# Kernel optimization log

Measured on AMD Instinct MI355X. Metric: run time of the kernel, lower is better.

Reference implementation:

```python
import jax, jax.numpy as jnp
import numpy as np

B, K, D = 65536, 1024, 256
COMMITMENT_COST = 0.25


def setup_inputs() -> dict:
    key = jax.random.key(0)
    kz, kw = jax.random.split(key)
    z = jax.random.normal(kz, (B, D), dtype=jnp.float32)
    # torch init: uniform_(-1/num_embeddings, 1/num_embeddings)
    weight = jax.random.uniform(kw, (K, D), dtype=jnp.float32,
                                minval=-1.0 / K, maxval=1.0 / K)
    return {"z": z, "weight": weight}


def reference(z, weight):
    # squared L2 distances via expansion: ||z||^2 - 2 z.e + ||e||^2  -> [B, K]
    dists = (jnp.sum(z * z, axis=1, keepdims=True)
             - 2.0 * (z @ weight.T)
             + jnp.sum(weight * weight, axis=1))
    indices = jnp.argmin(dists, axis=1)          # [B]
    z_q = weight[indices]                         # [B, D] gather

    sg_z = jax.lax.stop_gradient(z)
    mse = jnp.mean((z_q - sg_z) ** 2)
    commitment_loss = COMMITMENT_COST * mse      # F.mse_loss(z.detach(), z_q)
    vq_loss = mse + commitment_loss              # F.mse_loss(z_q, z.detach()) + commitment

    # straight-through estimator
    z_q_st = z + jax.lax.stop_gradient(z_q - z)
    return z_q_st, vq_loss, indices
```

## Files before the change

kernel.cpp:

```cpp
#include <hip/hip_runtime.h>
#include <math.h>

#define B_N 65536
#define K_N 1024
#define D_N 256
#define CAPW 512
#define NWV 8

typedef __attribute__((ext_vector_type(8))) short bf16x8;
typedef __attribute__((ext_vector_type(4))) float f32x4;

__device__ __forceinline__ unsigned short f2bf(float f) {
    unsigned u = __float_as_uint(f);
    return (unsigned short)((u + 0x7FFFu + ((u >> 16) & 1u)) >> 16);
}
__device__ __forceinline__ unsigned encf(float f) {
    unsigned u = __float_as_uint(f);
    return u ^ ((unsigned)((int)u >> 31) | 0x80000000u);
}
__device__ __forceinline__ float decf(unsigned e) {
    unsigned u = (e & 0x80000000u) ? (e ^ 0x80000000u) : ~e;
    return __uint_as_float(u);
}

__device__ __forceinline__ float chain_dot(const float* __restrict__ zp,
                                           const float* __restrict__ wp) {
    float acc = 0.0f;
    #pragma unroll 1
    for (int j = 0; j < 64; ++j) {
        float4 za = *reinterpret_cast<const float4*>(zp + (j << 2));
        float4 wa = *reinterpret_cast<const float4*>(wp + (j << 2));
        acc = fmaf(za.x, wa.x, acc);
        acc = fmaf(za.y, wa.y, acc);
        acc = fmaf(za.z, wa.z, acc);
        acc = fmaf(za.w, wa.w, acc);
    }
    return acc;
}

__device__ __forceinline__ int pA(int i, int k) {
    return ((i + k) & 15) - 7 + 9 * ((k >> 4) & 1);
}
__device__ __forceinline__ int pB(int j, int k) {
    return ((j + 3 * k) & 15) - 7 + 5 * ((k >> 4) & 1);
}

__global__ void mfma_probe_kernel(int* __restrict__ flag) {
    const int l = threadIdx.x & 63;
    const int c15 = l & 15, g = l >> 4;
    bf16x8 afr[8], bfr[8];
    #pragma unroll
    for (int m = 0; m < 8; ++m)
        #pragma unroll
        for (int e = 0; e < 8; ++e) {
            const int k = m * 32 + g * 8 + e;
            afr[m][e] = (short)f2bf((float)pA(c15, k));
            bfr[m][e] = (short)f2bf((float)pB(c15, k));
        }
    f32x4 acc = {0.f, 0.f, 0.f, 0.f};
    #pragma unroll
    for (int m = 0; m < 8; ++m)
        acc = __builtin_amdgcn_mfma_f32_16x16x32_bf16(afr[m], bfr[m], acc, 0, 0, 0);
    int h1 = 1, h2 = 1;
    #pragma unroll 1
    for (int reg = 0; reg < 4; ++reg) {
        const int q = 4 * g + reg;
        int e1 = 0, e2 = 0;
        for (int k = 0; k < 32; ++k) {
            e1 += pA(q, k) * pB(c15, k);
            e2 += pA(c15, k) * pB(q, k);
        }
        e1 *= 8; e2 *= 8;
        if (acc[reg] != (float)e1) h1 = 0;
        if (acc[reg] != (float)e2) h2 = 0;
    }
    h1 = __all(h1); h2 = __all(h2);
    if (threadIdx.x == 0) *flag = h1 ? 0 : (h2 ? 1 : 2);
}

__global__ void wprep_kernel(const float* __restrict__ w,
                             float* __restrict__ ww,
                             unsigned short* __restrict__ wb) {
    int wave = (int)((blockIdx.x * blockDim.x + threadIdx.x) >> 6);
    int lane = threadIdx.x & 63;
    if (wave >= K_N) return;
    const float4 v = *reinterpret_cast<const float4*>(w + ((size_t)wave << 8) + (lane << 2));
    float s = v.x * v.x + v.y * v.y + v.z * v.z + v.w * v.w;
    #pragma unroll
    for (int off = 32; off; off >>= 1) s += __shfl_xor(s, off, 64);
    if (lane == 0) ww[wave] = s;
    ushort4 b;
    b.x = f2bf(v.x); b.y = f2bf(v.y); b.z = f2bf(v.z); b.w = f2bf(v.w);
    const int mp = lane >> 3;
    const int gp = (lane >> 1) & 3;
    const int hp = (wave >> 4) & 1;
    const size_t off_b = (size_t)(wave >> 5) * 16384
        + (size_t)(((hp * 8 + mp) * 64 + gp * 16 + (wave & 15)) * 16)
        + (size_t)((lane & 1) * 8);
    *reinterpret_cast<ushort4*>((char*)wb + off_b) = b;
}

__global__ __launch_bounds__(512, 4)
void vq_mfma_kernel(const float* __restrict__ z, const float* __restrict__ w,
                    const unsigned short* __restrict__ wb,
                    const float* __restrict__ ww,
                    const int* __restrict__ flagp,
                    float* __restrict__ zq_out,
                    float* __restrict__ idxf_out,
                    double* __restrict__ partial) {
    __shared__ float wwlds[1024];
    __shared__ unsigned short rc[NWV][CAPW];
    __shared__ unsigned short dqv[NWV][CAPW];
    __shared__ float zz_l[NWV][16], band_l[NWV][16], thrm[NWV][16];
    __shared__ unsigned rowminU[NWV][16];
    __shared__ unsigned long long bestk[NWV][16];
    __shared__ double wsum[NWV];

    const int tid = threadIdx.x;
    const int wv = tid >> 6, l = tid & 63;
    const int c15 = l & 15, g = l >> 4;
    const int b0 = blockIdx.x << 7;
    const int rbase = b0 + (wv << 4);
    const int flag = flagp[0];
    const bool fb0 = !(flag == 0 || flag == 1);

    if (l < 16) {
        rowminU[wv][l] = 0xFFFFFFFFu;
        bestk[wv][l]   = ~0ull;
    }
    reinterpret_cast<float2*>(wwlds)[tid] = reinterpret_cast<const float2*>(ww)[tid];

    bool fbw = fb0;
    int n = 0;

    int ml[4], cl[4];
    #pragma unroll
    for (int reg = 0; reg < 4; ++reg) {
        if (flag == 1) { ml[reg] = c15;          cl[reg] = 4 * g + reg; }
        else           { ml[reg] = 4 * g + reg;  cl[reg] = c15;         }
    }

    bf16x8 afr[8];
    {
        const float* zr = z + ((size_t)(rbase + c15) << 8) + (g << 3);
        float s = 0.0f, a = 0.0f;
        #pragma unroll
        for (int m = 0; m < 8; ++m) {
            float4 lo = *reinterpret_cast<const float4*>(zr + (m << 5));
            float4 hi = *reinterpret_cast<const float4*>(zr + (m << 5) + 4);
            s += lo.x * lo.x + lo.y * lo.y + lo.z * lo.z + lo.w * lo.w;
            s += hi.x * hi.x + hi.y * hi.y + hi.z * hi.z + hi.w * hi.w;
            a += fabsf(lo.x) + fabsf(lo.y) + fabsf(lo.z) + fabsf(lo.w);
            a += fabsf(hi.x) + fabsf(hi.y) + fabsf(hi.z) + fabsf(hi.w);
            bf16x8 f;
            f[0] = (short)f2bf(lo.x); f[1] = (short)f2bf(lo.y);
            f[2] = (short)f2bf(lo.z); f[3] = (short)f2bf(lo.w);
            f[4] = (short)f2bf(hi.x); f[5] = (short)f2bf(hi.y);
            f[6] = (short)f2bf(hi.z); f[7] = (short)f2bf(hi.w);
            afr[m] = f;
        }
        s += __shfl_xor(s, 16, 64);
        s += __shfl_xor(s, 32, 64);
        a += __shfl_xor(a, 16, 64);
        a += __shfl_xor(a, 32, 64);
        if (g == 0) {
            zz_l[wv][c15]   = s;
            band_l[wv][c15] = a * 2.0e-5f + 1.0e-3f;
        }
    }

    __syncthreads();

    float zzv[4], bdv[4];
    #pragma unroll
    for (int reg = 0; reg < 4; ++reg) {
        zzv[reg] = zz_l[wv][ml[reg]];
        bdv[reg] = band_l[wv][ml[reg]];
    }

    float runmin[4] = {INFINITY, INFINITY, INFINITY, INFINITY};
    int base = 0;

    const char* wbL = (const char*)wb + (l << 4);

#define PROCESS(ACC, TC, DOCOL, DOFM)                                         \
    _Pragma("unroll")                                                         \
    for (int reg = 0; reg < 4; ++reg) {                                       \
        const int _code = ((TC) << 5) + (h << 4) + cl[reg];                   \
        const float _dist = (zzv[reg] - 2.0f * (ACC)[reg]) + wwlds[_code];    \
        if (DOCOL) {                                                          \
            const bool _pred = (_dist <= runmin[reg] + bdv[reg]);             \
            const unsigned long long _mask = __ballot(_pred);                 \
            if (_mask) {                                                      \
                if (_pred) {                                                  \
                    const int _slot = base + (int)__popcll(_mask & ((1ull << l) - 1ull)); \
                    if (_slot < CAPW) {                                       \
                        rc[wv][_slot] = (unsigned short)((ml[reg] << 10) | _code); \
                        union { _Float16 h16; unsigned short u; } _cv;        \
                        _cv.h16 = (_Float16)(_dist - zzv[reg]);               \
                        dqv[wv][_slot] = _cv.u;                               \
                    }                                                         \
                }                                                             \
                base += (int)__popcll(_mask);                                 \
            }                                                                 \
        }                                                                     \
        if (DOFM) runmin[reg] = fminf(runmin[reg], _dist);                    \
    }

#define MINSYNC()                                                             \
    if (flag == 1) {                                                          \
        _Pragma("unroll")                                                     \
        for (int reg = 0; reg < 4; ++reg) {                                   \
            runmin[reg] = fminf(runmin[reg], __shfl_xor(runmin[reg], 16, 64)); \
            runmin[reg] = fminf(runmin[reg], __shfl_xor(runmin[reg], 32, 64)); \
        }                                                                     \
    } else {                                                                  \
        _Pragma("unroll")                                                     \
        for (int reg = 0; reg < 4; ++reg) {                                   \
            runmin[reg] = fminf(runmin[reg], __shfl_xor(runmin[reg], 1, 64)); \
            runmin[reg] = fminf(runmin[reg], __shfl_xor(runmin[reg], 2, 64)); \
            runmin[reg] = fminf(runmin[reg], __shfl_xor(runmin[reg], 4, 64)); \
            runmin[reg] = fminf(runmin[reg], __shfl_xor(runmin[reg], 8, 64)); \
        }                                                                     \
    }

    if (!fb0) {
        #pragma unroll 1
        for (int t = 0; t < 32; ++t) {
            const char* tp = wbL + t * 16384;
            #pragma unroll
            for (int h = 0; h < 2; ++h) {
                bf16x8 bfr[8];
                #pragma unroll
                for (int m = 0; m < 8; ++m)
                    bfr[m] = *reinterpret_cast<const bf16x8*>(tp + (h << 13) + (m << 10));
                f32x4 acc = {0.f, 0.f, 0.f, 0.f};
                #pragma unroll
                for (int m = 0; m < 8; ++m)
                    acc = __builtin_amdgcn_mfma_f32_16x16x32_bf16(afr[m], bfr[m], acc, 0, 0, 0);
                if (t > 0) { PROCESS(acc, t, 1, 1) }
                else       { PROCESS(acc, t, 0, 1) }
            }
            MINSYNC()
        }

        {
            const char* tp = wbL;
            #pragma unroll
            for (int h = 0; h < 2; ++h) {
                bf16x8 bfr[8];
                #pragma unroll
                for (int m = 0; m < 8; ++m)
                    bfr[m] = *reinterpret_cast<const bf16x8*>(tp + (h << 13) + (m << 10));
                f32x4 acc = {0.f, 0.f, 0.f, 0.f};
                #pragma unroll
                for (int m = 0; m < 8; ++m)
                    acc = __builtin_amdgcn_mfma_f32_16x16x32_bf16(afr[m], bfr[m], acc, 0, 0, 0);
                PROCESS(acc, 0, 1, 0)
            }
        }

        n = base;
        if (n > CAPW) fbw = true;

        #pragma unroll
        for (int reg = 0; reg < 4; ++reg)
            atomicMin(&rowminU[wv][ml[reg]], encf(runmin[reg]));
        if (l < 16)
            thrm[wv][l] = (decf(rowminU[wv][l]) + band_l[wv][l]) - zz_l[wv][l] + 4.0e-4f;
    }
#undef PROCESS
#undef MINSYNC

    if (!fbw) {
        int viol = 0;
        #pragma unroll 1
        for (int i = l; i < n; i += 64) {
            const int e = rc[wv][i];
            const int m = e >> 10, code = e & 1023;
            union { _Float16 h16; unsigned short u; } cv;
            cv.u = dqv[wv][i];
            const float dval = (float)cv.h16;
            if (dval <= thrm[wv][m]) {
                const float dot = chain_dot(z + ((size_t)(rbase + m) << 8),
                                            w + ((size_t)code << 8));
                const float dist = (zz_l[wv][m] - 2.0f * dot) + wwlds[code];
                if (fabsf((dval + zz_l[wv][m]) - dist) > band_l[wv][m] + 4.0e-4f)
                    viol = 1;
                atomicMin(&bestk[wv][m],
                          ((unsigned long long)encf(dist) << 32) | (unsigned)code);
            }
        }
        if (__any(viol)) fbw = true;
    }
    if (fbw) {
        #pragma unroll 1
        for (int m = 0; m < 16; ++m) {
            const float zzm = zz_l[wv][m];
            const float* zp = z + ((size_t)(rbase + m) << 8);
            for (int code = l; code < 1024; code += 64) {
                const float dist = (zzm - 2.0f * chain_dot(zp, w + ((size_t)code << 8)))
                                 + wwlds[code];
                atomicMin(&bestk[wv][m],
                          ((unsigned long long)encf(dist) << 32) | (unsigned)code);
            }
        }
    }

    if (l < 16) {
        const int code = (int)(unsigned)(bestk[wv][l] & 0xFFFFFFFFull);
        idxf_out[rbase + l] = (float)code;
    }

    int codes[16];
    #pragma unroll
    for (int rr = 0; rr < 16; ++rr)
        codes[rr] = (int)(unsigned)(bestk[wv][rr] & 0xFFFFFFFFull);
    #pragma unroll 4
    for (int rr = 0; rr < 16; ++rr) {
        const float4 wv4 = *reinterpret_cast<const float4*>(
            w + ((size_t)codes[rr] << 8) + (l << 2));
        *reinterpret_cast<float4*>(
            zq_out + ((size_t)(rbase + rr) << 8) + (l << 2)) = wv4;
    }

    double s = 0.0;
    if (l < 16) s = (double)decf((unsigned)(bestk[wv][l] >> 32));
    #pragma unroll
    for (int off = 8; off; off >>= 1) s += __shfl_xor(s, off, 64);
    if (l == 0) wsum[wv] = s;
    __syncthreads();
    if (tid == 0) {
        double t = 0.0;
        #pragma unroll
        for (int i = 0; i < NWV; ++i) t += wsum[i];
        partial[blockIdx.x] = t;
    }
}

__global__ void finalize_loss_kernel(const double* __restrict__ partial,
                                     float* __restrict__ out) {
    __shared__ double sd[256];
    const int t = threadIdx.x;
    double s = 0.0;
    for (int i = t; i < 512; i += 256) s += partial[i];
    sd[t] = s;
    __syncthreads();
    #pragma unroll
    for (int off = 128; off; off >>= 1) {
        if (t < off) sd[t] += sd[t + off];
        __syncthreads();
    }
    if (t == 0) {
        double mse = sd[0] / ((double)B_N * (double)D_N);
        out[0] = (float)(mse * 1.25);
    }
}

extern "C" void kernel_launch(void* const* d_in, const int* in_sizes, int n_in,
                              void* d_out, int out_size, void* d_ws, size_t ws_size,
                              hipStream_t stream) {
    const float* z = (const float*)d_in[0];
    const float* w = (const float*)d_in[1];

    float* out  = (float*)d_out;
    float* zq   = out;
    float* loss = out + (size_t)B_N * D_N;
    float* idxf = loss + 1;

    char* wsb = (char*)d_ws;
    float*          ww      = (float*)(wsb);
    unsigned short* wb      = (unsigned short*)(wsb + 4096);
    int*            flag    = (int*)(wsb + 528384);
    double*         partial = (double*)(wsb + 528448);

    mfma_probe_kernel<<<1, 64, 0, stream>>>(flag);

    wprep_kernel<<<K_N / 4, 256, 0, stream>>>(w, ww, wb);

    vq_mfma_kernel<<<B_N / 128, 512, 0, stream>>>(z, w, wb, ww, flag,
                                                  zq, idxf, partial);

    finalize_loss_kernel<<<1, 256, 0, stream>>>(partial, loss);
}
```

Before: 188.9 us.

## Split codebook across wave pairs and halve rows per block

Each pair of waves now shares the same 16 z rows, with each wave scanning one half of the codebook. Per-row minimums and best codes are merged through shared-memory atomics, with added block barriers. Each block covers 64 rows, so the grid doubles to give more resident blocks per CU and better latency hiding. In exchange, each z row is loaded and converted to bf16 twice. The per-wave running minimum sees only half the codes, so the filter is looser and may keep more candidates.

```diff
diff --git a/kernel.cpp b/kernel.cpp
--- a/kernel.cpp
+++ b/kernel.cpp
@@ -111,22 +111,24 @@
     __shared__ float wwlds[1024];
     __shared__ unsigned short rc[NWV][CAPW];
     __shared__ unsigned short dqv[NWV][CAPW];
-    __shared__ float zz_l[NWV][16], band_l[NWV][16], thrm[NWV][16];
-    __shared__ unsigned rowminU[NWV][16];
-    __shared__ unsigned long long bestk[NWV][16];
-    __shared__ double wsum[NWV];
+    __shared__ float zz_l[4][16], band_l[4][16], thrm[4][16];
+    __shared__ unsigned rowminU[4][16];
+    __shared__ unsigned long long bestk[4][16];
+    __shared__ double wsum[4];
 
     const int tid = threadIdx.x;
     const int wv = tid >> 6, l = tid & 63;
+    const int wv2 = wv >> 1;
+    const int kh = wv & 1;
     const int c15 = l & 15, g = l >> 4;
-    const int b0 = blockIdx.x << 7;
-    const int rbase = b0 + (wv << 4);
+    const int b0 = blockIdx.x << 6;
+    const int rbase = b0 + (wv2 << 4);
     const int flag = flagp[0];
     const bool fb0 = !(flag == 0 || flag == 1);
 
-    if (l < 16) {
-        rowminU[wv][l] = 0xFFFFFFFFu;
-        bestk[wv][l]   = ~0ull;
+    if (kh == 0 && l < 16) {
+        rowminU[wv2][l] = 0xFFFFFFFFu;
+        bestk[wv2][l]   = ~0ull;
     }
     reinterpret_cast<float2*>(wwlds)[tid] = reinterpret_cast<const float2*>(ww)[tid];
 
@@ -164,8 +166,8 @@
         a += __shfl_xor(a, 16, 64);
         a += __shfl_xor(a, 32, 64);
         if (g == 0) {
-            zz_l[wv][c15]   = s;
-            band_l[wv][c15] = a * 2.0e-5f + 1.0e-3f;
+            zz_l[wv2][c15]   = s;
+            band_l[wv2][c15] = a * 2.0e-5f + 1.0e-3f;
         }
     }
 
@@ -174,19 +176,19 @@
     float zzv[4], bdv[4];
     #pragma unroll
     for (int reg = 0; reg < 4; ++reg) {
-        zzv[reg] = zz_l[wv][ml[reg]];
-        bdv[reg] = band_l[wv][ml[reg]];
+        zzv[reg] = zz_l[wv2][ml[reg]];
+        bdv[reg] = band_l[wv2][ml[reg]];
     }
 
     float runmin[4] = {INFINITY, INFINITY, INFINITY, INFINITY};
     int base = 0;
 
-    const char* wbL = (const char*)wb + (l << 4);
+    const char* wbL = (const char*)wb + (l << 4) + (kh << 13);
 
 #define PROCESS(ACC, TC, DOCOL, DOFM)                                         \
     _Pragma("unroll")                                                         \
     for (int reg = 0; reg < 4; ++reg) {                                       \
-        const int _code = ((TC) << 5) + (h << 4) + cl[reg];                   \
+        const int _code = ((TC) << 5) + (kh << 4) + cl[reg];                  \
         const float _dist = (zzv[reg] - 2.0f * (ACC)[reg]) + wwlds[_code];    \
         if (DOCOL) {                                                          \
             const bool _pred = (_dist <= runmin[reg] + bdv[reg]);             \
@@ -228,36 +230,29 @@
         #pragma unroll 1
         for (int t = 0; t < 32; ++t) {
             const char* tp = wbL + t * 16384;
+            bf16x8 bfr[8];
             #pragma unroll
-            for (int h = 0; h < 2; ++h) {
-                bf16x8 bfr[8];
-                #pragma unroll
-                for (int m = 0; m < 8; ++m)
-                    bfr[m] = *reinterpret_cast<const bf16x8*>(tp + (h << 13) + (m << 10));
-                f32x4 acc = {0.f, 0.f, 0.f, 0.f};
-                #pragma unroll
-                for (int m = 0; m < 8; ++m)
-                    acc = __builtin_amdgcn_mfma_f32_16x16x32_bf16(afr[m], bfr[m], acc, 0, 0, 0);
-                if (t > 0) { PROCESS(acc, t, 1, 1) }
-                else       { PROCESS(acc, t, 0, 1) }
-            }
+            for (int m = 0; m < 8; ++m)
+                bfr[m] = *reinterpret_cast<const bf16x8*>(tp + (m << 10));
+            f32x4 acc = {0.f, 0.f, 0.f, 0.f};
+            #pragma unroll
+            for (int m = 0; m < 8; ++m)
+                acc = __builtin_amdgcn_mfma_f32_16x16x32_bf16(afr[m], bfr[m], acc, 0, 0, 0);
+            if (t > 0) { PROCESS(acc, t, 1, 1) }
+            else       { PROCESS(acc, t, 0, 1) }
             MINSYNC()
         }
 
         {
-            const char* tp = wbL;
+            bf16x8 bfr[8];
             #pragma unroll
-            for (int h = 0; h < 2; ++h) {
-                bf16x8 bfr[8];
-                #pragma unroll
-                for (int m = 0; m < 8; ++m)
-                    bfr[m] = *reinterpret_cast<const bf16x8*>(tp + (h << 13) + (m << 10));
-                f32x4 acc = {0.f, 0.f, 0.f, 0.f};
-                #pragma unroll
-                for (int m = 0; m < 8; ++m)
-                    acc = __builtin_amdgcn_mfma_f32_16x16x32_bf16(afr[m], bfr[m], acc, 0, 0, 0);
-                PROCESS(acc, 0, 1, 0)
-            }
+            for (int m = 0; m < 8; ++m)
+                bfr[m] = *reinterpret_cast<const bf16x8*>(wbL + (m << 10));
+            f32x4 acc = {0.f, 0.f, 0.f, 0.f};
+            #pragma unroll
+            for (int m = 0; m < 8; ++m)
+                acc = __builtin_amdgcn_mfma_f32_16x16x32_bf16(afr[m], bfr[m], acc, 0, 0, 0);
+            PROCESS(acc, 0, 1, 0)
         }
 
         n = base;
@@ -265,9 +260,14 @@
 
         #pragma unroll
         for (int reg = 0; reg < 4; ++reg)
-            atomicMin(&rowminU[wv][ml[reg]], encf(runmin[reg]));
+            atomicMin(&rowminU[wv2][ml[reg]], encf(runmin[reg]));
+    }
+
+    __syncthreads();
+
+    if (!fb0) {
         if (l < 16)
-            thrm[wv][l] = (decf(rowminU[wv][l]) + band_l[wv][l]) - zz_l[wv][l] + 4.0e-4f;
+            thrm[wv2][l] = (decf(rowminU[wv2][l]) + band_l[wv2][l]) - zz_l[wv2][l] + 4.0e-4f;
     }
 #undef PROCESS
 #undef MINSYNC
@@ -281,13 +281,13 @@
             union { _Float16 h16; unsigned short u; } cv;
             cv.u = dqv[wv][i];
             const float dval = (float)cv.h16;
-            if (dval <= thrm[wv][m]) {
+            if (dval <= thrm[wv2][m]) {
                 const float dot = chain_dot(z + ((size_t)(rbase + m) << 8),
                                             w + ((size_t)code << 8));
-                const float dist = (zz_l[wv][m] - 2.0f * dot) + wwlds[code];
-                if (fabsf((dval + zz_l[wv][m]) - dist) > band_l[wv][m] + 4.0e-4f)
+                const float dist = (zz_l[wv2][m] - 2.0f * dot) + wwlds[code];
+                if (fabsf((dval + zz_l[wv2][m]) - dist) > band_l[wv2][m] + 4.0e-4f)
                     viol = 1;
-                atomicMin(&bestk[wv][m],
+                atomicMin(&bestk[wv2][m],
                           ((unsigned long long)encf(dist) << 32) | (unsigned)code);
             }
         }
@@ -296,44 +296,45 @@
     if (fbw) {
         #pragma unroll 1
         for (int m = 0; m < 16; ++m) {
-            const float zzm = zz_l[wv][m];
+            const float zzm = zz_l[wv2][m];
             const float* zp = z + ((size_t)(rbase + m) << 8);
             for (int code = l; code < 1024; code += 64) {
                 const float dist = (zzm - 2.0f * chain_dot(zp, w + ((size_t)code << 8)))
                                  + wwlds[code];
-                atomicMin(&bestk[wv][m],
+                atomicMin(&bestk[wv2][m],
                           ((unsigned long long)encf(dist) << 32) | (unsigned)code);
             }
         }
     }
 
-    if (l < 16) {
-        const int code = (int)(unsigned)(bestk[wv][l] & 0xFFFFFFFFull);
+    __syncthreads();
+
+    if (kh == 0 && l < 16) {
+        const int code = (int)(unsigned)(bestk[wv2][l] & 0xFFFFFFFFull);
         idxf_out[rbase + l] = (float)code;
     }
 
-    int codes[16];
-    #pragma unroll
-    for (int rr = 0; rr < 16; ++rr)
-        codes[rr] = (int)(unsigned)(bestk[wv][rr] & 0xFFFFFFFFull);
     #pragma unroll 4
-    for (int rr = 0; rr < 16; ++rr) {
+    for (int rr = kh * 8; rr < kh * 8 + 8; ++rr) {
+        const int code = (int)(unsigned)(bestk[wv2][rr] & 0xFFFFFFFFull);
         const float4 wv4 = *reinterpret_cast<const float4*>(
-            w + ((size_t)codes[rr] << 8) + (l << 2));
+            w + ((size_t)code << 8) + (l << 2));
         *reinterpret_cast<float4*>(
             zq_out + ((size_t)(rbase + rr) << 8) + (l << 2)) = wv4;
     }
 
-    double s = 0.0;
-    if (l < 16) s = (double)decf((unsigned)(bestk[wv][l] >> 32));
-    #pragma unroll
-    for (int off = 8; off; off >>= 1) s += __shfl_xor(s, off, 64);
-    if (l == 0) wsum[wv] = s;
+    if (kh == 0) {
+        double s = 0.0;
+        if (l < 16) s = (double)decf((unsigned)(bestk[wv2][l] >> 32));
+        #pragma unroll
+        for (int off = 8; off; off >>= 1) s += __shfl_xor(s, off, 64);
+        if (l == 0) wsum[wv2] = s;
+    }
     __syncthreads();
     if (tid == 0) {
         double t = 0.0;
         #pragma unroll
-        for (int i = 0; i < NWV; ++i) t += wsum[i];
+        for (int i = 0; i < 4; ++i) t += wsum[i];
         partial[blockIdx.x] = t;
     }
 }
@@ -343,7 +344,7 @@
     __shared__ double sd[256];
     const int t = threadIdx.x;
     double s = 0.0;
-    for (int i = t; i < 512; i += 256) s += partial[i];
+    for (int i = t; i < 1024; i += 256) s += partial[i];
     sd[t] = s;
     __syncthreads();
     #pragma unroll
@@ -378,8 +379,8 @@
 
     wprep_kernel<<<K_N / 4, 256, 0, stream>>>(w, ww, wb);
 
-    vq_mfma_kernel<<<B_N / 128, 512, 0, stream>>>(z, w, wb, ww, flag,
-                                                  zq, idxf, partial);
+    vq_mfma_kernel<<<B_N / 64, 512, 0, stream>>>(z, w, wb, ww, flag,
+                                                 zq, idxf, partial);
 
     finalize_loss_kernel<<<1, 256, 0, stream>>>(partial, loss);
 }
```

New measurement: 226.9 us. +20.2%, slower.
